# Kernel tuning notes

Hardware: AMD Instinct MI355X
Metric: run time of the kernel (lower is better)

The kernel has to match this reference:

```python
import jax, jax.numpy as jnp
import numpy as np

C, PH, PW, H, W = 10, 7, 7, 34, 34
STRIDE = 16.0  # heat_map_a
S = 4          # sample_per_part
P = PH * PW


def setup_inputs() -> dict:
    key = jax.random.key(0)
    k1, k2, k3, k4, k5 = jax.random.split(key, 5)
    N = 16384
    ft = jax.random.normal(k1, (1, C * PH * PW, H, W), dtype=jnp.float32)
    x1 = jax.random.uniform(k2, (N,), minval=0.0, maxval=400.0)
    y1 = jax.random.uniform(k3, (N,), minval=0.0, maxval=400.0)
    bw = jax.random.uniform(k4, (N,), minval=8.0, maxval=200.0)
    bh = jax.random.uniform(k5, (N,), minval=8.0, maxval=200.0)
    rois = jnp.stack([jnp.zeros((N,), jnp.float32), x1, y1, x1 + bw, y1 + bh], axis=1)
    return {"ft_add_left_right": ft, "rois": rois}


def _forward(ft_all, rois):
    ft = ft_all[0].reshape(C, PH, PW, H, W)
    roi_start_w = rois[:, 1] / STRIDE
    roi_start_h = rois[:, 2] / STRIDE
    roi_end_w = rois[:, 3] / STRIDE
    roi_end_h = rois[:, 4] / STRIDE
    roi_h = roi_end_h - roi_start_h
    roi_w = roi_end_w - roi_start_w
    # torch.threshold(x, 0.1, 0.1): keep x where x > 0.1 else 0.1
    roi_h = jnp.where(roi_h > 0.1, roi_h, 0.1)
    roi_w = jnp.where(roi_w > 0.1, roi_w, 0.1)
    bin_h = roi_h / PH
    bin_w = roi_w / PW
    sub_h = bin_h / S
    sub_w = bin_w / S
    gh, gw = jnp.meshgrid(jnp.arange(PH), jnp.arange(PW), indexing="ij")
    phs = gh.reshape(-1, 1)  # (P,1)
    pws = gw.reshape(-1, 1)
    hstart = jnp.floor(roi_start_h + phs * bin_h)  # (P,N)
    wstart = jnp.floor(roi_start_w + pws * bin_w)

    offs = jnp.asarray([[ih, iw] for ih in range(S) for iw in range(S)], dtype=jnp.float32)

    def gather(y, x):  # y,x: (P,N) int32 -> (C,P,N)
        return ft[:, phs, pws, y, x]

    def body(carry, off):
        sum_, count = carry
        w = wstart + (off[1] + 0.5) * sub_w  # (P,N)
        h = hstart + (off[0] + 0.5) * sub_h
        keep = (w > -1) & (w < W) & (h > -1) & (h < H)
        x1f = jnp.floor(w); x2f = jnp.ceil(w)
        y1f = jnp.floor(h); y2f = jnp.ceil(h)
        x1v = ((x1f >= 0) & (x1f < W)).astype(jnp.float32)
        x2v = ((x2f >= 0) & (x2f < W)).astype(jnp.float32)
        y1v = ((y1f >= 0) & (y1f < H)).astype(jnp.float32)
        y2v = ((y2f >= 0) & (y2f < H)).astype(jnp.float32)
        x1 = jnp.clip(x1f, 0, W - 1).astype(jnp.int32)
        x2 = jnp.clip(x2f, 0, W - 1).astype(jnp.int32)
        y1 = jnp.clip(y1f, 0, H - 1).astype(jnp.int32)
        y2 = jnp.clip(y2f, 0, H - 1).astype(jnp.int32)
        dx = w - x1.astype(jnp.float32)
        dy = h - y1.astype(jnp.float32)
        v11 = gather(y1, x1) * (x1v * y1v)
        v12 = gather(y2, x1) * (x1v * y2v)
        v21 = gather(y1, x2) * (x2v * y1v)
        v22 = gather(y2, x2) * (x2v * y2v)
        value = ((1 - dx) * (1 - dy) * v11 + (1 - dx) * dy * v12
                 + dx * (1 - dy) * v21 + dx * dy * v22)
        kf = keep.astype(jnp.float32)
        return (sum_ + value * kf, count + kf), None

    N = rois.shape[0]
    init = (jnp.zeros((C, P, N), jnp.float32), jnp.zeros((P, N), jnp.float32))
    (sum_, count), _ = jax.lax.scan(body, init, offs)
    out = sum_ / jnp.where(count > 0, count, 1.0)
    return out.transpose(2, 0, 1)  # (N, C, P)


def reference(ft_add_left_right, rois):
    return _forward(ft_add_left_right, rois)
```

## Files before the change

### kernel.cpp

```cpp
#include <hip/hip_runtime.h>


constexpr int C  = 10;
constexpr int PH = 7;
constexpr int PW = 7;
constexpr int H  = 34;
constexpr int W  = 34;
constexpr int P  = PH * PW;
constexpr int HW = H * W;
constexpr int FT_C_STRIDE = P * HW;
constexpr int CP = 12;
constexpr int R  = C * P;
constexpr int NB = 16;

__global__ __launch_bounds__(256) void dfmb_swizzle(
    const float* __restrict__ ft, float* __restrict__ ftT)
{
    const int p = blockIdx.x;
    const int c = blockIdx.y;
    const float* __restrict__ src = ft + (size_t)c * FT_C_STRIDE + p * HW;
    float* __restrict__ dst = ftT + (size_t)p * (HW * CP) + c;
    for (int pix = threadIdx.x; pix < HW; pix += 256)
        dst[(size_t)pix * CP] = src[pix];
}

__global__ __launch_bounds__(256, 4) void dfmb_fused(
    const float* __restrict__ ftT,
    const float* __restrict__ rois,
    float* __restrict__ out,
    int N)
{
    __shared__ float olds[NB * R];

    const int n0 = blockIdx.x * NB;

    for (int k = 0; k < 4; ++k) {
        const int j = threadIdx.x + k * 256;
        if (j < P * NB) {
            const int p     = j >> 4;
            const int n_loc = j & 15;
            const int n     = n0 + n_loc;
            const int ph = p / PW;
            const int pw = p - ph * PW;

            float wstart, hstart, sub_w, sub_h;
            {
#pragma clang fp contract(off)
                const float inv_stride = 0.0625f;
                float rsw = rois[n * 5 + 1] * inv_stride;
                float rsh = rois[n * 5 + 2] * inv_stride;
                float rew = rois[n * 5 + 3] * inv_stride;
                float reh = rois[n * 5 + 4] * inv_stride;
                float roi_h = reh - rsh; if (!(roi_h > 0.1f)) roi_h = 0.1f;
                float roi_w = rew - rsw; if (!(roi_w > 0.1f)) roi_w = 0.1f;
                float bin_h = roi_h / 7.0f;
                float bin_w = roi_w / 7.0f;
                sub_h = bin_h * 0.25f;
                sub_w = bin_w * 0.25f;
                hstart = floorf(rsh + (float)ph * bin_h);
                wstart = floorf(rsw + (float)pw * bin_w);
            }

            float Xw0 = 0.f, Xw1 = 0.f, Xw2 = 0.f, Xw3 = 0.f, cntx = 0.f;
            int xbase = 0;
#pragma unroll
            for (int iw = 0; iw < 4; ++iw) {
                float w;
                {
#pragma clang fp contract(off)
                    w = wstart + ((float)iw + 0.5f) * sub_w;
                }
                float kw  = (w > -1.0f && w < 34.0f) ? 1.0f : 0.0f;
                float x1f = floorf(w), x2f = ceilf(w);
                float x1v = (x1f >= 0.0f && x1f < 34.0f) ? 1.0f : 0.0f;
                float x2v = (x2f >= 0.0f && x2f < 34.0f) ? 1.0f : 0.0f;
                int x1 = (int)fminf(fmaxf(x1f, 0.0f), 33.0f);
                int x2 = (int)fminf(fmaxf(x2f, 0.0f), 33.0f);
                float dx = w - (float)x1;
                if (iw == 0) xbase = x1;
                float a = kw * (1.0f - dx) * x1v;
                float b = kw * dx * x2v;
                int i1 = x1 - xbase, i2 = x2 - xbase;
                Xw0 += (i1 == 0) ? a : 0.f;  Xw1 += (i1 == 1) ? a : 0.f;
                Xw2 += (i1 == 2) ? a : 0.f;  Xw3 += (i1 == 3) ? a : 0.f;
                Xw0 += (i2 == 0) ? b : 0.f;  Xw1 += (i2 == 1) ? b : 0.f;
                Xw2 += (i2 == 2) ? b : 0.f;  Xw3 += (i2 == 3) ? b : 0.f;
                cntx += kw;
            }

            float Yw0 = 0.f, Yw1 = 0.f, Yw2 = 0.f, Yw3 = 0.f, cnty = 0.f;
            int ybase = 0;
#pragma unroll
            for (int ih = 0; ih < 4; ++ih) {
                float h;
                {
#pragma clang fp contract(off)
                    h = hstart + ((float)ih + 0.5f) * sub_h;
                }
                float kh  = (h > -1.0f && h < 34.0f) ? 1.0f : 0.0f;
                float y1f = floorf(h), y2f = ceilf(h);
                float y1v = (y1f >= 0.0f && y1f < 34.0f) ? 1.0f : 0.0f;
                float y2v = (y2f >= 0.0f && y2f < 34.0f) ? 1.0f : 0.0f;
                int y1 = (int)fminf(fmaxf(y1f, 0.0f), 33.0f);
                int y2 = (int)fminf(fmaxf(y2f, 0.0f), 33.0f);
                float dy = h - (float)y1;
                if (ih == 0) ybase = y1;
                float a = kh * (1.0f - dy) * y1v;
                float b = kh * dy * y2v;
                int i1 = y1 - ybase, i2 = y2 - ybase;
                Yw0 += (i1 == 0) ? a : 0.f;  Yw1 += (i1 == 1) ? a : 0.f;
                Yw2 += (i1 == 2) ? a : 0.f;  Yw3 += (i1 == 3) ? a : 0.f;
                Yw0 += (i2 == 0) ? b : 0.f;  Yw1 += (i2 == 1) ? b : 0.f;
                Yw2 += (i2 == 2) ? b : 0.f;  Yw3 += (i2 == 3) ? b : 0.f;
                cnty += kh;
            }

            const float* __restrict__ slab = ftT + (size_t)p * (HW * CP);
            float4 s0 = {0.f, 0.f, 0.f, 0.f};
            float4 s1 = {0.f, 0.f, 0.f, 0.f};
            float2 s2 = {0.f, 0.f};
#pragma unroll
            for (int cy = 0; cy < 4; ++cy) {
                float wy = (cy == 0) ? Yw0 : (cy == 1) ? Yw1 : (cy == 2) ? Yw2 : Yw3;
                if (wy != 0.0f) {
                    int yy = min(ybase + cy, 33);
                    const float* rowp = slab + yy * (W * CP);
#pragma unroll
                    for (int cx = 0; cx < 4; ++cx) {
                        float wx = (cx == 0) ? Xw0 : (cx == 1) ? Xw1
                                 : (cx == 2) ? Xw2 : Xw3;
                        float wgt = wy * wx;
                        if (wgt != 0.0f) {
                            int xx = min(xbase + cx, 33);
                            const float* t = rowp + xx * CP;
                            float4 v0 = *(const float4*)(t);
                            float4 v1 = *(const float4*)(t + 4);
                            float2 v2 = *(const float2*)(t + 8);
                            s0.x += wgt * v0.x; s0.y += wgt * v0.y;
                            s0.z += wgt * v0.z; s0.w += wgt * v0.w;
                            s1.x += wgt * v1.x; s1.y += wgt * v1.y;
                            s1.z += wgt * v1.z; s1.w += wgt * v1.w;
                            s2.x += wgt * v2.x; s2.y += wgt * v2.y;
                        }
                    }
                }
            }

            float cnt = cntx * cnty;
            if (!(cnt > 0.0f)) cnt = 1.0f;
            float inv = 1.0f / cnt;

            float* __restrict__ ol = olds + n_loc * R + p;
            ol[0 * P] = s0.x * inv;  ol[1 * P] = s0.y * inv;
            ol[2 * P] = s0.z * inv;  ol[3 * P] = s0.w * inv;
            ol[4 * P] = s1.x * inv;  ol[5 * P] = s1.y * inv;
            ol[6 * P] = s1.z * inv;  ol[7 * P] = s1.w * inv;
            ol[8 * P] = s2.x * inv;  ol[9 * P] = s2.y * inv;
        }
    }

    __syncthreads();

    float4* __restrict__ dst4 = (float4*)(out + (size_t)n0 * R);
    const float4* __restrict__ src4 = (const float4*)olds;
    for (int i = threadIdx.x; i < (NB * R) / 4; i += 256)
        dst4[i] = src4[i];
}

__global__ __launch_bounds__(512, 4) void dfmb_phase1_direct(
    const float* __restrict__ ft,
    const float* __restrict__ rois,
    float* __restrict__ dst,
    int N)
{
    __shared__ float tile[HW * CP];
    const int p  = blockIdx.y;
    const int ph = p / PW;
    const int pw = p - ph * PW;
    const float* __restrict__ src = ft + p * HW;
    for (int i = threadIdx.x; i < C * HW; i += 512) {
        int c = i / HW;
        int r = i - c * HW;
        tile[r * CP + c] = src[c * FT_C_STRIDE + r];
    }
    __syncthreads();
    const int n = blockIdx.x * 512 + threadIdx.x;
    if (n >= N) return;
    float wstart, hstart, sub_w, sub_h;
    {
#pragma clang fp contract(off)
        const float inv_stride = 0.0625f;
        float rsw = rois[n * 5 + 1] * inv_stride;
        float rsh = rois[n * 5 + 2] * inv_stride;
        float rew = rois[n * 5 + 3] * inv_stride;
        float reh = rois[n * 5 + 4] * inv_stride;
        float roi_h = reh - rsh; if (!(roi_h > 0.1f)) roi_h = 0.1f;
        float roi_w = rew - rsw; if (!(roi_w > 0.1f)) roi_w = 0.1f;
        float bin_h = roi_h / 7.0f;
        float bin_w = roi_w / 7.0f;
        sub_h = bin_h * 0.25f;
        sub_w = bin_w * 0.25f;
        hstart = floorf(rsh + (float)ph * bin_h);
        wstart = floorf(rsw + (float)pw * bin_w);
    }
    float Xw[4] = {0,0,0,0}, Yw[4] = {0,0,0,0};
    float cntx = 0.f, cnty = 0.f;
    int xbase = 0, ybase = 0;
#pragma unroll
    for (int iw = 0; iw < 4; ++iw) {
        float w;
        {
#pragma clang fp contract(off)
            w = wstart + ((float)iw + 0.5f) * sub_w;
        }
        float kw  = (w > -1.0f && w < 34.0f) ? 1.0f : 0.0f;
        float x1f = floorf(w), x2f = ceilf(w);
        float x1v = (x1f >= 0.0f && x1f < 34.0f) ? 1.0f : 0.0f;
        float x2v = (x2f >= 0.0f && x2f < 34.0f) ? 1.0f : 0.0f;
        int x1 = (int)fminf(fmaxf(x1f, 0.0f), 33.0f);
        int x2 = (int)fminf(fmaxf(x2f, 0.0f), 33.0f);
        float dx = w - (float)x1;
        if (iw == 0) xbase = x1;
        Xw[x1 - xbase] += kw * (1.0f - dx) * x1v;
        Xw[x2 - xbase] += kw * dx * x2v;
        cntx += kw;
    }
#pragma unroll
    for (int ih = 0; ih < 4; ++ih) {
        float h;
        {
#pragma clang fp contract(off)
            h = hstart + ((float)ih + 0.5f) * sub_h;
        }
        float kh  = (h > -1.0f && h < 34.0f) ? 1.0f : 0.0f;
        float y1f = floorf(h), y2f = ceilf(h);
        float y1v = (y1f >= 0.0f && y1f < 34.0f) ? 1.0f : 0.0f;
        float y2v = (y2f >= 0.0f && y2f < 34.0f) ? 1.0f : 0.0f;
        int y1 = (int)fminf(fmaxf(y1f, 0.0f), 33.0f);
        int y2 = (int)fminf(fmaxf(y2f, 0.0f), 33.0f);
        float dy = h - (float)y1;
        if (ih == 0) ybase = y1;
        Yw[y1 - ybase] += kh * (1.0f - dy) * y1v;
        Yw[y2 - ybase] += kh * dy * y2v;
        cnty += kh;
    }
    float4 s0 = {0,0,0,0}, s1 = {0,0,0,0};
    float2 s2 = {0,0};
#pragma unroll
    for (int cy = 0; cy < 4; ++cy) {
        if (Yw[cy] != 0.0f) {
            int yy = min(ybase + cy, 33);
            const float* rowp = &tile[yy * (W * CP)];
#pragma unroll
            for (int cx = 0; cx < 4; ++cx) {
                float wgt = Yw[cy] * Xw[cx];
                if (wgt != 0.0f) {
                    int xx = min(xbase + cx, 33);
                    const float* t = rowp + xx * CP;
                    float4 v0 = *(const float4*)(t);
                    float4 v1 = *(const float4*)(t + 4);
                    float2 v2 = *(const float2*)(t + 8);
                    s0.x += wgt * v0.x; s0.y += wgt * v0.y;
                    s0.z += wgt * v0.z; s0.w += wgt * v0.w;
                    s1.x += wgt * v1.x; s1.y += wgt * v1.y;
                    s1.z += wgt * v1.z; s1.w += wgt * v1.w;
                    s2.x += wgt * v2.x; s2.y += wgt * v2.y;
                }
            }
        }
    }
    float cnt = cntx * cnty;
    if (!(cnt > 0.0f)) cnt = 1.0f;
    float inv = 1.0f / cnt;
    float r[10] = { s0.x*inv, s0.y*inv, s0.z*inv, s0.w*inv,
                    s1.x*inv, s1.y*inv, s1.z*inv, s1.w*inv,
                    s2.x*inv, s2.y*inv };
    float* __restrict__ o = dst + (size_t)n * R + p;
#pragma unroll
    for (int c = 0; c < C; ++c) o[c * P] = r[c];
}

extern "C" void kernel_launch(void* const* d_in, const int* in_sizes, int n_in,
                              void* d_out, int out_size, void* d_ws, size_t ws_size,
                              hipStream_t stream) {
    const float* ft   = (const float*)d_in[0];
    const float* rois = (const float*)d_in[1];
    float* out = (float*)d_out;
    const int N = in_sizes[1] / 5;

    const size_t need = (size_t)P * HW * CP * sizeof(float);
    if (d_ws != nullptr && ws_size >= need && (N % NB) == 0) {
        float* ftT = (float*)d_ws;
        dfmb_swizzle<<<dim3(P, C), dim3(256), 0, stream>>>(ft, ftT);
        dfmb_fused<<<dim3(N / NB), dim3(256), 0, stream>>>(ftT, rois, out, N);
    } else {
        dim3 grid1((N + 511) / 512, P);
        dfmb_phase1_direct<<<grid1, dim3(512), 0, stream>>>(ft, rois, out, N);
    }
}
```

Before: 103.7 us.

## Pack features as bf16 in LDS slabs and transpose output in separate pass

Pre-packs the feature map into bf16 pairs per pixel so that a whole per-part slab (34x34x12 halves) fits in shared memory. The main kernel now runs one block per (N-tile, part), reading samples from LDS instead of global memory. It writes to a coalesced N-minor workspace, and a third kernel transposes that into the (N, C, P) output. This cuts gather bandwidth and latency but adds bf16 rounding error on the feature values, an extra kernel launch, and a full round trip of the output through the workspace.

```diff
diff --git a/kernel.cpp b/kernel.cpp
--- a/kernel.cpp
+++ b/kernel.cpp
@@ -9,183 +9,61 @@
 constexpr int P  = PH * PW;
 constexpr int HW = H * W;
 constexpr int FT_C_STRIDE = P * HW;
-constexpr int CP = 12;
+constexpr int SPX = 12;
+constexpr int SLAB_US = HW * SPX;
+constexpr int CPAD = 12;
 constexpr int R  = C * P;
-constexpr int NB = 16;
-
-__global__ __launch_bounds__(256) void dfmb_swizzle(
-    const float* __restrict__ ft, float* __restrict__ ftT)
+
+__device__ inline unsigned bf16rn(float f) {
+    unsigned u = __float_as_uint(f);
+    return (u + 0x7FFFu + ((u >> 16) & 1u)) >> 16;
+}
+__device__ inline float bf16lo(unsigned u) { return __uint_as_float(u << 16); }
+__device__ inline float bf16hi(unsigned u) { return __uint_as_float(u & 0xFFFF0000u); }
+
+__global__ __launch_bounds__(256) void dfmb_pack(
+    const float* __restrict__ ft, ushort* __restrict__ ftB)
 {
     const int p = blockIdx.x;
-    const int c = blockIdx.y;
-    const float* __restrict__ src = ft + (size_t)c * FT_C_STRIDE + p * HW;
-    float* __restrict__ dst = ftT + (size_t)p * (HW * CP) + c;
-    for (int pix = threadIdx.x; pix < HW; pix += 256)
-        dst[(size_t)pix * CP] = src[pix];
-}
-
-__global__ __launch_bounds__(256, 4) void dfmb_fused(
-    const float* __restrict__ ftT,
+    const float* __restrict__ src = ft + p * HW;
+    for (int pix = threadIdx.x; pix < HW; pix += 256) {
+        unsigned d[6];
+#pragma unroll
+        for (int k = 0; k < 5; ++k) {
+            float a = src[(2 * k) * FT_C_STRIDE + pix];
+            float b = src[(2 * k + 1) * FT_C_STRIDE + pix];
+            d[k] = bf16rn(a) | (bf16rn(b) << 16);
+        }
+        d[5] = 0;
+        uint2* dst = (uint2*)(ftB + (size_t)p * SLAB_US + pix * SPX);
+        dst[0] = make_uint2(d[0], d[1]);
+        dst[1] = make_uint2(d[2], d[3]);
+        dst[2] = make_uint2(d[4], d[5]);
+    }
+}
+
+__global__ __launch_bounds__(256, 5) void dfmb_main(
+    const ushort* __restrict__ ftB,
     const float* __restrict__ rois,
-    float* __restrict__ out,
+    float* __restrict__ ws,
     int N)
 {
-    __shared__ float olds[NB * R];
-
-    const int n0 = blockIdx.x * NB;
-
-    for (int k = 0; k < 4; ++k) {
-        const int j = threadIdx.x + k * 256;
-        if (j < P * NB) {
-            const int p     = j >> 4;
-            const int n_loc = j & 15;
-            const int n     = n0 + n_loc;
-            const int ph = p / PW;
-            const int pw = p - ph * PW;
-
-            float wstart, hstart, sub_w, sub_h;
-            {
-#pragma clang fp contract(off)
-                const float inv_stride = 0.0625f;
-                float rsw = rois[n * 5 + 1] * inv_stride;
-                float rsh = rois[n * 5 + 2] * inv_stride;
-                float rew = rois[n * 5 + 3] * inv_stride;
-                float reh = rois[n * 5 + 4] * inv_stride;
-                float roi_h = reh - rsh; if (!(roi_h > 0.1f)) roi_h = 0.1f;
-                float roi_w = rew - rsw; if (!(roi_w > 0.1f)) roi_w = 0.1f;
-                float bin_h = roi_h / 7.0f;
-                float bin_w = roi_w / 7.0f;
-                sub_h = bin_h * 0.25f;
-                sub_w = bin_w * 0.25f;
-                hstart = floorf(rsh + (float)ph * bin_h);
-                wstart = floorf(rsw + (float)pw * bin_w);
-            }
-
-            float Xw0 = 0.f, Xw1 = 0.f, Xw2 = 0.f, Xw3 = 0.f, cntx = 0.f;
-            int xbase = 0;
-#pragma unroll
-            for (int iw = 0; iw < 4; ++iw) {
-                float w;
-                {
-#pragma clang fp contract(off)
-                    w = wstart + ((float)iw + 0.5f) * sub_w;
-                }
-                float kw  = (w > -1.0f && w < 34.0f) ? 1.0f : 0.0f;
-                float x1f = floorf(w), x2f = ceilf(w);
-                float x1v = (x1f >= 0.0f && x1f < 34.0f) ? 1.0f : 0.0f;
-                float x2v = (x2f >= 0.0f && x2f < 34.0f) ? 1.0f : 0.0f;
-                int x1 = (int)fminf(fmaxf(x1f, 0.0f), 33.0f);
-                int x2 = (int)fminf(fmaxf(x2f, 0.0f), 33.0f);
-                float dx = w - (float)x1;
-                if (iw == 0) xbase = x1;
-                float a = kw * (1.0f - dx) * x1v;
-                float b = kw * dx * x2v;
-                int i1 = x1 - xbase, i2 = x2 - xbase;
-                Xw0 += (i1 == 0) ? a : 0.f;  Xw1 += (i1 == 1) ? a : 0.f;
-                Xw2 += (i1 == 2) ? a : 0.f;  Xw3 += (i1 == 3) ? a : 0.f;
-                Xw0 += (i2 == 0) ? b : 0.f;  Xw1 += (i2 == 1) ? b : 0.f;
-                Xw2 += (i2 == 2) ? b : 0.f;  Xw3 += (i2 == 3) ? b : 0.f;
-                cntx += kw;
-            }
-
-            float Yw0 = 0.f, Yw1 = 0.f, Yw2 = 0.f, Yw3 = 0.f, cnty = 0.f;
-            int ybase = 0;
-#pragma unroll
-            for (int ih = 0; ih < 4; ++ih) {
-                float h;
-                {
-#pragma clang fp contract(off)
-                    h = hstart + ((float)ih + 0.5f) * sub_h;
-                }
-                float kh  = (h > -1.0f && h < 34.0f) ? 1.0f : 0.0f;
-                float y1f = floorf(h), y2f = ceilf(h);
-                float y1v = (y1f >= 0.0f && y1f < 34.0f) ? 1.0f : 0.0f;
-                float y2v = (y2f >= 0.0f && y2f < 34.0f) ? 1.0f : 0.0f;
-                int y1 = (int)fminf(fmaxf(y1f, 0.0f), 33.0f);
-                int y2 = (int)fminf(fmaxf(y2f, 0.0f), 33.0f);
-                float dy = h - (float)y1;
-                if (ih == 0) ybase = y1;
-                float a = kh * (1.0f - dy) * y1v;
-                float b = kh * dy * y2v;
-                int i1 = y1 - ybase, i2 = y2 - ybase;
-                Yw0 += (i1 == 0) ? a : 0.f;  Yw1 += (i1 == 1) ? a : 0.f;
-                Yw2 += (i1 == 2) ? a : 0.f;  Yw3 += (i1 == 3) ? a : 0.f;
-                Yw0 += (i2 == 0) ? b : 0.f;  Yw1 += (i2 == 1) ? b : 0.f;
-                Yw2 += (i2 == 2) ? b : 0.f;  Yw3 += (i2 == 3) ? b : 0.f;
-                cnty += kh;
-            }
-
-            const float* __restrict__ slab = ftT + (size_t)p * (HW * CP);
-            float4 s0 = {0.f, 0.f, 0.f, 0.f};
-            float4 s1 = {0.f, 0.f, 0.f, 0.f};
-            float2 s2 = {0.f, 0.f};
-#pragma unroll
-            for (int cy = 0; cy < 4; ++cy) {
-                float wy = (cy == 0) ? Yw0 : (cy == 1) ? Yw1 : (cy == 2) ? Yw2 : Yw3;
-                if (wy != 0.0f) {
-                    int yy = min(ybase + cy, 33);
-                    const float* rowp = slab + yy * (W * CP);
-#pragma unroll
-                    for (int cx = 0; cx < 4; ++cx) {
-                        float wx = (cx == 0) ? Xw0 : (cx == 1) ? Xw1
-                                 : (cx == 2) ? Xw2 : Xw3;
-                        float wgt = wy * wx;
-                        if (wgt != 0.0f) {
-                            int xx = min(xbase + cx, 33);
-                            const float* t = rowp + xx * CP;
-                            float4 v0 = *(const float4*)(t);
-                            float4 v1 = *(const float4*)(t + 4);
-                            float2 v2 = *(const float2*)(t + 8);
-                            s0.x += wgt * v0.x; s0.y += wgt * v0.y;
-                            s0.z += wgt * v0.z; s0.w += wgt * v0.w;
-                            s1.x += wgt * v1.x; s1.y += wgt * v1.y;
-                            s1.z += wgt * v1.z; s1.w += wgt * v1.w;
-                            s2.x += wgt * v2.x; s2.y += wgt * v2.y;
-                        }
-                    }
-                }
-            }
-
-            float cnt = cntx * cnty;
-            if (!(cnt > 0.0f)) cnt = 1.0f;
-            float inv = 1.0f / cnt;
-
-            float* __restrict__ ol = olds + n_loc * R + p;
-            ol[0 * P] = s0.x * inv;  ol[1 * P] = s0.y * inv;
-            ol[2 * P] = s0.z * inv;  ol[3 * P] = s0.w * inv;
-            ol[4 * P] = s1.x * inv;  ol[5 * P] = s1.y * inv;
-            ol[6 * P] = s1.z * inv;  ol[7 * P] = s1.w * inv;
-            ol[8 * P] = s2.x * inv;  ol[9 * P] = s2.y * inv;
-        }
-    }
-
-    __syncthreads();
-
-    float4* __restrict__ dst4 = (float4*)(out + (size_t)n0 * R);
-    const float4* __restrict__ src4 = (const float4*)olds;
-    for (int i = threadIdx.x; i < (NB * R) / 4; i += 256)
-        dst4[i] = src4[i];
-}
-
-__global__ __launch_bounds__(512, 4) void dfmb_phase1_direct(
-    const float* __restrict__ ft,
-    const float* __restrict__ rois,
-    float* __restrict__ dst,
-    int N)
-{
-    __shared__ float tile[HW * CP];
+    __shared__ ushort slab[SLAB_US];
+
     const int p  = blockIdx.y;
     const int ph = p / PW;
     const int pw = p - ph * PW;
-    const float* __restrict__ src = ft + p * HW;
-    for (int i = threadIdx.x; i < C * HW; i += 512) {
-        int c = i / HW;
-        int r = i - c * HW;
-        tile[r * CP + c] = src[c * FT_C_STRIDE + r];
+
+    {
+        const uint4* __restrict__ s4 = (const uint4*)(ftB + (size_t)p * SLAB_US);
+        uint4* d4 = (uint4*)slab;
+        for (int i = threadIdx.x; i < SLAB_US / 8; i += 256) d4[i] = s4[i];
     }
     __syncthreads();
-    const int n = blockIdx.x * 512 + threadIdx.x;
+
+    const int n = blockIdx.x * 256 + threadIdx.x;
     if (n >= N) return;
+
     float wstart, hstart, sub_w, sub_h;
     {
 #pragma clang fp contract(off)
@@ -203,9 +81,9 @@
         hstart = floorf(rsh + (float)ph * bin_h);
         wstart = floorf(rsw + (float)pw * bin_w);
     }
-    float Xw[4] = {0,0,0,0}, Yw[4] = {0,0,0,0};
-    float cntx = 0.f, cnty = 0.f;
-    int xbase = 0, ybase = 0;
+
+    float Xw0 = 0.f, Xw1 = 0.f, Xw2 = 0.f, Xw3 = 0.f, cntx = 0.f;
+    int xbase = 0;
 #pragma unroll
     for (int iw = 0; iw < 4; ++iw) {
         float w;
@@ -221,10 +99,18 @@
         int x2 = (int)fminf(fmaxf(x2f, 0.0f), 33.0f);
         float dx = w - (float)x1;
         if (iw == 0) xbase = x1;
-        Xw[x1 - xbase] += kw * (1.0f - dx) * x1v;
-        Xw[x2 - xbase] += kw * dx * x2v;
+        float a = kw * (1.0f - dx) * x1v;
+        float b = kw * dx * x2v;
+        int i1 = x1 - xbase, i2 = x2 - xbase;
+        Xw0 += (i1 == 0) ? a : 0.f;  Xw1 += (i1 == 1) ? a : 0.f;
+        Xw2 += (i1 == 2) ? a : 0.f;  Xw3 += (i1 == 3) ? a : 0.f;
+        Xw0 += (i2 == 0) ? b : 0.f;  Xw1 += (i2 == 1) ? b : 0.f;
+        Xw2 += (i2 == 2) ? b : 0.f;  Xw3 += (i2 == 3) ? b : 0.f;
         cntx += kw;
     }
+
+    float Yw0 = 0.f, Yw1 = 0.f, Yw2 = 0.f, Yw3 = 0.f, cnty = 0.f;
+    int ybase = 0;
 #pragma unroll
     for (int ih = 0; ih < 4; ++ih) {
         float h;
@@ -240,41 +126,194 @@
         int y2 = (int)fminf(fmaxf(y2f, 0.0f), 33.0f);
         float dy = h - (float)y1;
         if (ih == 0) ybase = y1;
-        Yw[y1 - ybase] += kh * (1.0f - dy) * y1v;
-        Yw[y2 - ybase] += kh * dy * y2v;
+        float a = kh * (1.0f - dy) * y1v;
+        float b = kh * dy * y2v;
+        int i1 = y1 - ybase, i2 = y2 - ybase;
+        Yw0 += (i1 == 0) ? a : 0.f;  Yw1 += (i1 == 1) ? a : 0.f;
+        Yw2 += (i1 == 2) ? a : 0.f;  Yw3 += (i1 == 3) ? a : 0.f;
+        Yw0 += (i2 == 0) ? b : 0.f;  Yw1 += (i2 == 1) ? b : 0.f;
+        Yw2 += (i2 == 2) ? b : 0.f;  Yw3 += (i2 == 3) ? b : 0.f;
         cnty += kh;
     }
-    float4 s0 = {0,0,0,0}, s1 = {0,0,0,0};
-    float2 s2 = {0,0};
+
+    float s0=0.f,s1=0.f,s2=0.f,s3=0.f,s4=0.f,s5=0.f,s6=0.f,s7=0.f,s8=0.f,s9=0.f;
 #pragma unroll
     for (int cy = 0; cy < 4; ++cy) {
-        if (Yw[cy] != 0.0f) {
+        float wy = (cy == 0) ? Yw0 : (cy == 1) ? Yw1 : (cy == 2) ? Yw2 : Yw3;
+        if (wy != 0.0f) {
             int yy = min(ybase + cy, 33);
-            const float* rowp = &tile[yy * (W * CP)];
+            const ushort* rowp = slab + yy * (W * SPX);
 #pragma unroll
             for (int cx = 0; cx < 4; ++cx) {
-                float wgt = Yw[cy] * Xw[cx];
+                float wx = (cx == 0) ? Xw0 : (cx == 1) ? Xw1
+                         : (cx == 2) ? Xw2 : Xw3;
+                float wgt = wy * wx;
                 if (wgt != 0.0f) {
                     int xx = min(xbase + cx, 33);
-                    const float* t = rowp + xx * CP;
-                    float4 v0 = *(const float4*)(t);
-                    float4 v1 = *(const float4*)(t + 4);
-                    float2 v2 = *(const float2*)(t + 8);
-                    s0.x += wgt * v0.x; s0.y += wgt * v0.y;
-                    s0.z += wgt * v0.z; s0.w += wgt * v0.w;
-                    s1.x += wgt * v1.x; s1.y += wgt * v1.y;
-                    s1.z += wgt * v1.z; s1.w += wgt * v1.w;
-                    s2.x += wgt * v2.x; s2.y += wgt * v2.y;
+                    const uint2* t = (const uint2*)(rowp + xx * SPX);
+                    uint2 a = t[0], b = t[1], c2 = t[2];
+                    s0 += wgt * bf16lo(a.x);  s1 += wgt * bf16hi(a.x);
+                    s2 += wgt * bf16lo(a.y);  s3 += wgt * bf16hi(a.y);
+                    s4 += wgt * bf16lo(b.x);  s5 += wgt * bf16hi(b.x);
+                    s6 += wgt * bf16lo(b.y);  s7 += wgt * bf16hi(b.y);
+                    s8 += wgt * bf16lo(c2.x); s9 += wgt * bf16hi(c2.x);
                 }
             }
         }
     }
+
     float cnt = cntx * cnty;
     if (!(cnt > 0.0f)) cnt = 1.0f;
     float inv = 1.0f / cnt;
-    float r[10] = { s0.x*inv, s0.y*inv, s0.z*inv, s0.w*inv,
-                    s1.x*inv, s1.y*inv, s1.z*inv, s1.w*inv,
-                    s2.x*inv, s2.y*inv };
+    float r[10] = { s0*inv, s1*inv, s2*inv, s3*inv, s4*inv,
+                    s5*inv, s6*inv, s7*inv, s8*inv, s9*inv };
+
+    float* __restrict__ o = ws + (size_t)(n >> 6) * (R * 64)
+                               + (size_t)p * 64 + (n & 63);
+#pragma unroll
+    for (int c = 0; c < C; ++c) o[(size_t)(c * P) * 64] = r[c];
+}
+
+constexpr int TR = 245;
+__global__ __launch_bounds__(1024) void dfmb_phase2(
+    const float* __restrict__ ws, float* __restrict__ out, int N)
+{
+    __shared__ float t[TR * 65];
+    const int nblk = blockIdx.x;
+    const int r0   = blockIdx.y * TR;
+    const float* __restrict__ srcb = ws + (size_t)nblk * (R * 64) + (size_t)r0 * 64;
+
+    for (int i = threadIdx.x; i < TR * 16; i += 1024) {
+        int rr  = i >> 4;
+        int nl4 = (i & 15) * 4;
+        float4 v = ((const float4*)srcb)[i];
+        float* tp = &t[rr * 65 + nl4];
+        tp[0] = v.x; tp[1] = v.y; tp[2] = v.z; tp[3] = v.w;
+    }
+    __syncthreads();
+
+    const int n0 = nblk * 64;
+    for (int i = threadIdx.x; i < 64 * TR; i += 1024) {
+        int nl = i / TR;
+        int r  = i - nl * TR;
+        out[(size_t)(n0 + nl) * R + r0 + r] = t[r * 65 + nl];
+    }
+}
+
+__global__ __launch_bounds__(512, 4) void dfmb_phase1_direct(
+    const float* __restrict__ ft,
+    const float* __restrict__ rois,
+    float* __restrict__ dst,
+    int N)
+{
+    __shared__ float tile[HW * CPAD];
+    const int p  = blockIdx.y;
+    const int ph = p / PW;
+    const int pw = p - ph * PW;
+    const float* __restrict__ src = ft + p * HW;
+    for (int i = threadIdx.x; i < C * HW; i += 512) {
+        int c = i / HW;
+        int r = i - c * HW;
+        tile[r * CPAD + c] = src[c * FT_C_STRIDE + r];
+    }
+    __syncthreads();
+    const int n = blockIdx.x * 512 + threadIdx.x;
+    if (n >= N) return;
+    float wstart, hstart, sub_w, sub_h;
+    {
+#pragma clang fp contract(off)
+        const float inv_stride = 0.0625f;
+        float rsw = rois[n * 5 + 1] * inv_stride;
+        float rsh = rois[n * 5 + 2] * inv_stride;
+        float rew = rois[n * 5 + 3] * inv_stride;
+        float reh = rois[n * 5 + 4] * inv_stride;
+        float roi_h = reh - rsh; if (!(roi_h > 0.1f)) roi_h = 0.1f;
+        float roi_w = rew - rsw; if (!(roi_w > 0.1f)) roi_w = 0.1f;
+        float bin_h = roi_h / 7.0f;
+        float bin_w = roi_w / 7.0f;
+        sub_h = bin_h * 0.25f;
+        sub_w = bin_w * 0.25f;
+        hstart = floorf(rsh + (float)ph * bin_h);
+        wstart = floorf(rsw + (float)pw * bin_w);
+    }
+    float Xw0=0.f,Xw1=0.f,Xw2=0.f,Xw3=0.f,cntx=0.f;
+    float Yw0=0.f,Yw1=0.f,Yw2=0.f,Yw3=0.f,cnty=0.f;
+    int xbase = 0, ybase = 0;
+#pragma unroll
+    for (int iw = 0; iw < 4; ++iw) {
+        float w;
+        {
+#pragma clang fp contract(off)
+            w = wstart + ((float)iw + 0.5f) * sub_w;
+        }
+        float kw  = (w > -1.0f && w < 34.0f) ? 1.0f : 0.0f;
+        float x1f = floorf(w), x2f = ceilf(w);
+        float x1v = (x1f >= 0.0f && x1f < 34.0f) ? 1.0f : 0.0f;
+        float x2v = (x2f >= 0.0f && x2f < 34.0f) ? 1.0f : 0.0f;
+        int x1 = (int)fminf(fmaxf(x1f, 0.0f), 33.0f);
+        int x2 = (int)fminf(fmaxf(x2f, 0.0f), 33.0f);
+        float dx = w - (float)x1;
+        if (iw == 0) xbase = x1;
+        float a = kw * (1.0f - dx) * x1v;
+        float b = kw * dx * x2v;
+        int i1 = x1 - xbase, i2 = x2 - xbase;
+        Xw0 += (i1==0)?a:0.f; Xw1 += (i1==1)?a:0.f; Xw2 += (i1==2)?a:0.f; Xw3 += (i1==3)?a:0.f;
+        Xw0 += (i2==0)?b:0.f; Xw1 += (i2==1)?b:0.f; Xw2 += (i2==2)?b:0.f; Xw3 += (i2==3)?b:0.f;
+        cntx += kw;
+    }
+#pragma unroll
+    for (int ih = 0; ih < 4; ++ih) {
+        float h;
+        {
+#pragma clang fp contract(off)
+            h = hstart + ((float)ih + 0.5f) * sub_h;
+        }
+        float kh  = (h > -1.0f && h < 34.0f) ? 1.0f : 0.0f;
+        float y1f = floorf(h), y2f = ceilf(h);
+        float y1v = (y1f >= 0.0f && y1f < 34.0f) ? 1.0f : 0.0f;
+        float y2v = (y2f >= 0.0f && y2f < 34.0f) ? 1.0f : 0.0f;
+        int y1 = (int)fminf(fmaxf(y1f, 0.0f), 33.0f);
+        int y2 = (int)fminf(fmaxf(y2f, 0.0f), 33.0f);
+        float dy = h - (float)y1;
+        if (ih == 0) ybase = y1;
+        float a = kh * (1.0f - dy) * y1v;
+        float b = kh * dy * y2v;
+        int i1 = y1 - ybase, i2 = y2 - ybase;
+        Yw0 += (i1==0)?a:0.f; Yw1 += (i1==1)?a:0.f; Yw2 += (i1==2)?a:0.f; Yw3 += (i1==3)?a:0.f;
+        Yw0 += (i2==0)?b:0.f; Yw1 += (i2==1)?b:0.f; Yw2 += (i2==2)?b:0.f; Yw3 += (i2==3)?b:0.f;
+        cnty += kh;
+    }
+    float4 v0s = {0,0,0,0}, v1s = {0,0,0,0};
+    float2 v2s = {0,0};
+#pragma unroll
+    for (int cy = 0; cy < 4; ++cy) {
+        float wy = (cy==0)?Yw0:(cy==1)?Yw1:(cy==2)?Yw2:Yw3;
+        if (wy != 0.0f) {
+            int yy = min(ybase + cy, 33);
+            const float* rowp = &tile[yy * (W * CPAD)];
+#pragma unroll
+            for (int cx = 0; cx < 4; ++cx) {
+                float wx = (cx==0)?Xw0:(cx==1)?Xw1:(cx==2)?Xw2:Xw3;
+                float wgt = wy * wx;
+                if (wgt != 0.0f) {
+                    int xx = min(xbase + cx, 33);
+                    const float* t = rowp + xx * CPAD;
+                    float4 a = *(const float4*)(t);
+                    float4 b = *(const float4*)(t + 4);
+                    float2 c2 = *(const float2*)(t + 8);
+                    v0s.x += wgt*a.x; v0s.y += wgt*a.y; v0s.z += wgt*a.z; v0s.w += wgt*a.w;
+                    v1s.x += wgt*b.x; v1s.y += wgt*b.y; v1s.z += wgt*b.z; v1s.w += wgt*b.w;
+                    v2s.x += wgt*c2.x; v2s.y += wgt*c2.y;
+                }
+            }
+        }
+    }
+    float cnt = cntx * cnty;
+    if (!(cnt > 0.0f)) cnt = 1.0f;
+    float inv = 1.0f / cnt;
+    float r[10] = { v0s.x*inv, v0s.y*inv, v0s.z*inv, v0s.w*inv,
+                    v1s.x*inv, v1s.y*inv, v1s.z*inv, v1s.w*inv,
+                    v2s.x*inv, v2s.y*inv };
     float* __restrict__ o = dst + (size_t)n * R + p;
 #pragma unroll
     for (int c = 0; c < C; ++c) o[c * P] = r[c];
@@ -288,11 +327,15 @@
     float* out = (float*)d_out;
     const int N = in_sizes[1] / 5;
 
-    const size_t need = (size_t)P * HW * CP * sizeof(float);
-    if (d_ws != nullptr && ws_size >= need && (N % NB) == 0) {
-        float* ftT = (float*)d_ws;
-        dfmb_swizzle<<<dim3(P, C), dim3(256), 0, stream>>>(ft, ftT);
-        dfmb_fused<<<dim3(N / NB), dim3(256), 0, stream>>>(ftT, rois, out, N);
+    const size_t packB = (size_t)P * SLAB_US * sizeof(ushort);
+    const size_t wsOff = (packB + 255) & ~(size_t)255;
+    const size_t need  = wsOff + (size_t)R * N * sizeof(float);
+    if (d_ws != nullptr && ws_size >= need && (N % 256) == 0) {
+        ushort* ftB = (ushort*)d_ws;
+        float*  ws2 = (float*)((char*)d_ws + wsOff);
+        dfmb_pack<<<dim3(P), dim3(256), 0, stream>>>(ft, ftB);
+        dfmb_main<<<dim3(N / 256, P), dim3(256), 0, stream>>>(ftB, rois, ws2, N);
+        dfmb_phase2<<<dim3(N / 64, 2), dim3(1024), 0, stream>>>(ws2, out, N);
     } else {
         dim3 grid1((N + 511) / 512, P);
         dfmb_phase1_direct<<<grid1, dim3(512), 0, stream>>>(ft, rois, out, N);
```

After: 101.5 us. 2.1% less time.
